# Kernel tuning notes

Measured on AMD Instinct MI355X. Metric: run time of the kernel, lower is better.

## Reference

```python
import jax, jax.numpy as jnp
import numpy as np

N_ATOMS = 50000
DEG = 16
N_EDGES = N_ATOMS * DEG
N_MOL = 1000
NA = 23  # NUMBER_ATOMIC_GRAPH_FEATURES
NB = 7   # NUMBER_BOND_GRAPH_FEATURES


def _sph(v):
    # e3nn-style real spherical harmonics, lmax=2, normalize=False, 'component' normalization
    x, y, z = v[:, 0], v[:, 1], v[:, 2]
    sh1 = jnp.sqrt(3.0) * jnp.stack([x, y, z], axis=-1)  # [E,3] (1o)
    sh2 = jnp.stack([
        jnp.sqrt(15.0) * x * y,
        jnp.sqrt(15.0) * y * z,
        (jnp.sqrt(5.0) / 2.0) * (2 * z * z - x * x - y * y),
        jnp.sqrt(15.0) * x * z,
        (jnp.sqrt(15.0) / 2.0) * (x * x - y * y),
    ], axis=-1)  # [E,5] (2e)
    return sh1, sh2


def setup_inputs() -> dict:
    key = jax.random.key(0)
    ks = jax.random.split(key, 10)
    positions = jax.random.normal(ks[0], (N_ATOMS, 3), jnp.float32)
    x = jax.random.normal(ks[1], (N_ATOMS, NA), jnp.float32)
    edge_attr = jax.random.uniform(ks[2], (N_EDGES, NB), jnp.float32)
    edge_src = jax.random.randint(ks[3], (N_EDGES,), 0, N_ATOMS)
    edge_dst = jnp.repeat(jnp.arange(N_ATOMS), DEG)  # every node has in-degree DEG (required by the module)
    batch = jnp.repeat(jnp.arange(N_MOL), N_ATOMS // N_MOL)
    # tp1: FullyConnectedTensorProduct(NAx0e, 7x0e+7x1o+7x2e -> 32x0e+12x1e+12x1o+8x2e+8x2o)
    # allowed paths: 0e*0e->0e (32), 0e*1o->1o (12), 0e*2e->2e (8); 1e/2o outputs have no path (zero)
    W1_0 = jax.random.normal(ks[4], (NA, NB, 32), jnp.float32)
    W1_1 = jax.random.normal(ks[5], (NA, NB, 12), jnp.float32)
    W1_2 = jax.random.normal(ks[6], (NA, NB, 8), jnp.float32)
    # tp2: paths into 0e: 0e*0e (32x7), 1o*1o (12x7), 2e*2e (8x7)
    W2_0 = jax.random.normal(ks[7], (32, NB, 1), jnp.float32)
    W2_1 = jax.random.normal(ks[8], (12, NB, 1), jnp.float32)
    W2_2 = jax.random.normal(ks[9], (8, NB, 1), jnp.float32)
    return {"positions": positions, "x": x, "edge_attr": edge_attr,
            "W1_0": W1_0, "W1_1": W1_1, "W1_2": W1_2,
            "W2_0": W2_0, "W2_1": W2_1, "W2_2": W2_2,
            "edge_src": edge_src, "edge_dst": edge_dst, "batch": batch}


def reference(positions, x, edge_attr, W1_0, W1_1, W1_2, W2_0, W2_1, W2_2, edge_src, edge_dst, batch):
    N = x.shape[0]
    E = edge_attr.shape[0]
    M = N_MOL
    vec = positions[edge_src] - positions[edge_dst]            # [E,3]
    sh1, sh2 = _sph(vec)
    # FullTensorProduct(7x0e, 0e+1o+2e): scalar block is edge_attr itself; l>0 blocks are outer products
    b1 = edge_attr[:, :, None] * sh1[:, None, :]               # [E,NB,3]
    b2 = edge_attr[:, :, None] * sh2[:, None, :]               # [E,NB,5]
    deg = jax.ops.segment_sum(jnp.ones((E,), positions.dtype), edge_dst, num_segments=N)
    inv_sqrt_deg = 1.0 / jnp.sqrt(deg)                          # all nodes have >=1 edge by construction
    # tp1 on gathered source atom scalars. Since in1 is all-scalar, the SH factor separates:
    t = x[edge_src][:, :, None] * edge_attr[:, None, :]         # [E,NA,NB]
    n1 = 1.0 / np.sqrt(NA * NB)                                 # fan-in normalization
    m0 = jnp.einsum('eab,abo->eo', t, W1_0) * n1                # [E,32] 0e
    m1 = (jnp.einsum('eab,abo->eo', t, W1_1) * n1)[:, :, None] * sh1[:, None, :]  # [E,12,3] 1o
    m2 = (jnp.einsum('eab,abo->eo', t, W1_2) * n1)[:, :, None] * sh2[:, None, :]  # [E,8,5] 2e
    # (tp1's 12x1e and 8x2o outputs are structurally zero and have no path into tp2's 0e output -> dropped)
    s0 = jax.ops.segment_sum(m0, edge_dst, num_segments=N) * inv_sqrt_deg[:, None]
    s1 = jax.ops.segment_sum(m1, edge_dst, num_segments=N) * inv_sqrt_deg[:, None, None]
    s2 = jax.ops.segment_sum(m2, edge_dst, num_segments=N) * inv_sqrt_deg[:, None, None]
    # tp2 -> single 0e; l x l -> 0 contraction is inner product / sqrt(2l+1)
    e0 = jnp.einsum('ea,eb,ab->e', s0[edge_src], edge_attr, W2_0[:, :, 0]) / np.sqrt(32 * NB)
    e1 = jnp.einsum('eam,ebm,ab->e', s1[edge_src], b1, W2_1[:, :, 0]) / (np.sqrt(12 * NB) * np.sqrt(3.0))
    e2 = jnp.einsum('eam,ebm,ab->e', s2[edge_src], b2, W2_2[:, :, 0]) / (np.sqrt(8 * NB) * np.sqrt(5.0))
    edge_out = (e0 + e1 + e2)[:, None]                          # [E,1]
    node_out = jax.ops.segment_sum(edge_out, edge_dst, num_segments=N) * inv_sqrt_deg[:, None]
    apm = jax.ops.segment_sum(jnp.ones((N,), positions.dtype), batch, num_segments=M)
    acc = jax.ops.segment_sum(node_out, batch, num_segments=M)  # [M,1]
    return acc / jnp.sqrt(apm)[:, None]
```

## Files before the change

kernel.cpp:

```cpp
#include <hip/hip_runtime.h>
#include <hip/hip_bf16.h>

#define N_ATOMS 50000
#define DEG 16
#define N_MOL 1000
#define NA 23
#define NB 7
#define O0 32
#define O1 12
#define O2 8
#define OT 52
#define SROW 128
#define NPW 4
#define WFRAG_N 1792

typedef __attribute__((ext_vector_type(8))) short short8;
typedef __attribute__((ext_vector_type(4))) float floatx4;

__device__ __forceinline__ unsigned short bfbits(float f) {
    unsigned u = __float_as_uint(f);
    u += 0x7FFFu + ((u >> 16) & 1u);
    return (unsigned short)(u >> 16);
}
__device__ __forceinline__ float bf_lo(unsigned u) { return __uint_as_float(u << 16); }
__device__ __forceinline__ float bf_hi(unsigned u) { return __uint_as_float(u & 0xFFFF0000u); }
__device__ __forceinline__ float wred4(float v) {
    v += __shfl_xor(v, 16, 64); v += __shfl_xor(v, 32, 64); return v;
}

__global__ void k_prep(const float* __restrict__ W1_0, const float* __restrict__ W1_1,
                       const float* __restrict__ W1_2, const float* __restrict__ x,
                       const float* __restrict__ pos,
                       unsigned short* __restrict__ Wfrag,
                       unsigned short* __restrict__ x_bf, float4* __restrict__ pos4,
                       float* __restrict__ out) {
    int idx = blockIdx.x * 256 + threadIdx.x;
    if (idx < N_MOL) out[idx] = 0.0f;
    if (idx < WFRAG_N * 8) {
        int j    = idx & 7;
        int lane = (idx >> 3) & 63;
        int st   = idx >> 9;
        int s = st >> 2, t = st & 3;
        int a = (lane >> 4) * 8 + j, o = t * 16 + (lane & 15);
        float val = 0.f;
        if (a < NA && o < OT) {
            const float n1 = 0.07881104062391006f;
            if (o < O0)           val = W1_0[(a * NB + s) * O0 + o] * n1;
            else if (o < O0 + O1) val = W1_1[(a * NB + s) * O1 + (o - O0)] * n1;
            else                  val = W1_2[(a * NB + s) * O2 + (o - O0 - O1)] * n1;
        }
        Wfrag[idx] = bfbits(val);
    }
    if (idx < N_ATOMS) {
        float4 p; p.x = pos[idx * 3 + 0]; p.y = pos[idx * 3 + 1];
        p.z = pos[idx * 3 + 2]; p.w = 0.f;
        pos4[idx] = p;
    }
    if (idx < N_ATOMS * 32) {
        int n = idx >> 5, a = idx & 31;
        x_bf[idx] = bfbits((a < NA) ? x[n * NA + a] : 0.f);
    }
}

__global__ __launch_bounds__(256, 5) void k2_s(const float4* __restrict__ pos4,
        const unsigned short* __restrict__ x_bf, const float* __restrict__ edge_attr,
        const int* __restrict__ edge_src, const unsigned short* __restrict__ Wfrag,
        unsigned short* __restrict__ sbuf) {
    __shared__ short8 wfrag[WFRAG_N];
    __shared__ float hbuf[4][16][8];
    const int tid  = threadIdx.x;
    const int wid  = tid >> 6;
    const int lane = tid & 63;
    const int lcol = lane & 15;
    const int quad = lane >> 4;

    {
        uint4* dst = (uint4*)wfrag;
        const uint4* src4 = (const uint4*)Wfrag;
        for (int i = tid; i < WFRAG_N; i += 256) dst[i] = src4[i];
    }
    __syncthreads();

    const int wgid = __builtin_amdgcn_readfirstlane(blockIdx.x * 4 + wid);
    const int base = wgid * NPW;
    if (base >= N_ATOMS) return;

    float (*hb)[8] = hbuf[wid];
    const float s3 = 1.7320508075688772f, s15 = 3.872983346207417f;
    const float s5h = 1.118033988749895f, s15h = 1.9364916731037085f;

    auto clampn = [&](int i) { int nn = base + i; return nn < N_ATOMS ? nn : N_ATOMS - 1; };
    int s0v = edge_src[clampn(0) * DEG + lcol];
    int s1v = edge_src[clampn(1) * DEG + lcol];
    uint4 xu0 = *(const uint4*)(x_bf + s0v * 32 + quad * 8);
    float4 pp0 = pos4[s0v];
    float e0v[NB];
    {
        const float* p = edge_attr + ((size_t)clampn(0) * DEG + lcol) * NB;
        #pragma unroll
        for (int b = 0; b < NB; b++) e0v[b] = p[b];
    }

    #pragma unroll 1
    for (int i = 0; i < NPW; i++) {
        const int n = base + i;
        if (n >= N_ATOMS) break;
        int s2v = edge_src[clampn(i + 2 < NPW ? i + 2 : i) * DEG + lcol];
        uint4 xu1 = *(const uint4*)(x_bf + s1v * 32 + quad * 8);
        float4 pp1 = pos4[s1v];
        float e1v[NB];
        {
            const float* p = edge_attr + ((size_t)clampn(i + 1 < NPW ? i + 1 : i) * DEG + lcol) * NB;
            #pragma unroll
            for (int b = 0; b < NB; b++) e1v[b] = p[b];
        }
        float xf[8];
        xf[0] = bf_lo(xu0.x); xf[1] = bf_hi(xu0.x);
        xf[2] = bf_lo(xu0.y); xf[3] = bf_hi(xu0.y);
        xf[4] = bf_lo(xu0.z); xf[5] = bf_hi(xu0.z);
        xf[6] = bf_lo(xu0.w); xf[7] = bf_hi(xu0.w);

        const float4 pd = pos4[n];
        if (lane < 16) {
            const float vx = pp0.x - pd.x, vy = pp0.y - pd.y, vz = pp0.z - pd.z;
            hb[lane][0] = s3 * vx;  hb[lane][1] = s3 * vy;  hb[lane][2] = s3 * vz;
            hb[lane][3] = s15 * vx * vy;
            hb[lane][4] = s15 * vy * vz;
            hb[lane][5] = s5h * (2.f * vz * vz - vx * vx - vy * vy);
            hb[lane][6] = s15 * vx * vz;
            hb[lane][7] = s15h * (vx * vx - vy * vy);
        }
        floatx4 acc0 = {0.f,0.f,0.f,0.f}, acc1 = {0.f,0.f,0.f,0.f};
        floatx4 acc2 = {0.f,0.f,0.f,0.f}, acc3 = {0.f,0.f,0.f,0.f};
        #pragma unroll
        for (int s = 0; s < 7; s++) {
            const float eb = e0v[s];
            union { short8 v; unsigned u[4]; } af;
            #pragma unroll
            for (int j = 0; j < 8; j += 2) {
                float2 pr; pr.x = xf[j] * eb; pr.y = xf[j + 1] * eb;
                __hip_bfloat162 bb = __float22bfloat162_rn(pr);
                af.u[j >> 1] = *(unsigned*)&bb;
            }
            acc0 = __builtin_amdgcn_mfma_f32_16x16x32_bf16(af.v, wfrag[(s*4+0)*64 + lane], acc0, 0, 0, 0);
            acc1 = __builtin_amdgcn_mfma_f32_16x16x32_bf16(af.v, wfrag[(s*4+1)*64 + lane], acc1, 0, 0, 0);
            acc2 = __builtin_amdgcn_mfma_f32_16x16x32_bf16(af.v, wfrag[(s*4+2)*64 + lane], acc2, 0, 0, 0);
            acc3 = __builtin_amdgcn_mfma_f32_16x16x32_bf16(af.v, wfrag[(s*4+3)*64 + lane], acc3, 0, 0, 0);
        }
        float4 hA[4], hB[4];
        #pragma unroll
        for (int r = 0; r < 4; r++) {
            int e = quad * 4 + r;
            hA[r] = *(const float4*)&hb[e][0];
            hB[r] = *(const float4*)&hb[e][4];
        }
        const float q = 0.25f;
        unsigned short* sr = sbuf + (size_t)n * SROW;
        float v0 = wred4(acc0[0] + acc0[1] + acc0[2] + acc0[3]);
        float v1 = wred4(acc1[0] + acc1[1] + acc1[2] + acc1[3]);
        if (quad == 0) { sr[lcol] = bfbits(v0 * q); sr[16 + lcol] = bfbits(v1 * q); }
        if (lcol < 12) {
            float t0 = 0.f, t1 = 0.f, t2 = 0.f;
            #pragma unroll
            for (int r = 0; r < 4; r++) {
                float m = acc2[r];
                t0 += m * hA[r].x; t1 += m * hA[r].y; t2 += m * hA[r].z;
            }
            t0 = wred4(t0); t1 = wred4(t1); t2 = wred4(t2);
            if (quad == 0) {
                sr[32 + lcol] = bfbits(t0 * q);
                sr[44 + lcol] = bfbits(t1 * q);
                sr[56 + lcol] = bfbits(t2 * q);
            }
        } else {
            int a = lcol - 12;
            float t0 = 0.f, t1 = 0.f, t2 = 0.f, t3 = 0.f, t4 = 0.f;
            #pragma unroll
            for (int r = 0; r < 4; r++) {
                float m = acc2[r];
                t0 += m * hA[r].w; t1 += m * hB[r].x; t2 += m * hB[r].y;
                t3 += m * hB[r].z; t4 += m * hB[r].w;
            }
            t0 = wred4(t0); t1 = wred4(t1); t2 = wred4(t2); t3 = wred4(t3); t4 = wred4(t4);
            if (quad == 0) {
                sr[68 + a] = bfbits(t0 * q); sr[76 + a] = bfbits(t1 * q);
                sr[84 + a] = bfbits(t2 * q); sr[92 + a] = bfbits(t3 * q);
                sr[100 + a] = bfbits(t4 * q);
            }
        }
        if (lcol < 4) {
            int a = lcol + 4;
            float t0 = 0.f, t1 = 0.f, t2 = 0.f, t3 = 0.f, t4 = 0.f;
            #pragma unroll
            for (int r = 0; r < 4; r++) {
                float m = acc3[r];
                t0 += m * hA[r].w; t1 += m * hB[r].x; t2 += m * hB[r].y;
                t3 += m * hB[r].z; t4 += m * hB[r].w;
            }
            t0 = wred4(t0); t1 = wred4(t1); t2 = wred4(t2); t3 = wred4(t3); t4 = wred4(t4);
            if (quad == 0) {
                sr[68 + a] = bfbits(t0 * q); sr[76 + a] = bfbits(t1 * q);
                sr[84 + a] = bfbits(t2 * q); sr[92 + a] = bfbits(t3 * q);
                sr[100 + a] = bfbits(t4 * q);
            }
        }
        s0v = s1v; s1v = s2v;
        xu0 = xu1; pp0 = pp1;
        #pragma unroll
        for (int b = 0; b < NB; b++) e0v[b] = e1v[b];
    }
}

__global__ __launch_bounds__(256, 7) void k3_fused(const float4* __restrict__ pos4,
        const float* __restrict__ edge_attr, const int* __restrict__ edge_src,
        const unsigned short* __restrict__ sbuf,
        const float* __restrict__ W2_0, const float* __restrict__ W2_1,
        const float* __restrict__ W2_2, float* __restrict__ out) {
    __shared__ float ea_t[4][4][16][8];
    __shared__ float hbf[4][4][161];
    const int tid  = threadIdx.x;
    const int wid  = tid >> 6;
    const int lane = tid & 63;
    const int q    = lane >> 4;
    const int e    = lane & 15;
    const int base = __builtin_amdgcn_readfirstlane(blockIdx.x * 4 + wid) * 4;

    const float c0 = 0.06681531047810609f;
    const float c1 = 0.06299407883487121f;
    const float c2 = 0.05976143046671968f;
    int code = 0, aA = 0, aB = 0, valid = 1;
    const float* Wb = W2_0; float norm = c0;
    const int j = lane;
    if (j < 16)      { code = 0; aA = 2 * j;   aB = aA + 1; Wb = W2_0; norm = c0; }
    else if (j < 34) { int g = (j - 16) / 6, r = (j - 16) - 6 * g;
                       code = 1 + g; aA = 2 * r; aB = aA + 1; Wb = W2_1; norm = c1; }
    else if (j < 54) { int g = (j - 34) >> 2, r = (j - 34) & 3;
                       code = 4 + g; aA = 2 * r; aB = aA + 1; Wb = W2_2; norm = c2; }
    else             { valid = 0; }
    float wA[NB], wB[NB];
    #pragma unroll
    for (int b = 0; b < NB; b++) {
        wA[b] = valid ? Wb[aA * NB + b] * norm : 0.f;
        wB[b] = valid ? Wb[aB * NB + b] * norm : 0.f;
    }
    const int jj = valid ? j : 0;

    {
        const int nq = base + q;
        const int sE = edge_src[nq * DEG + e];
        const float* eap = edge_attr + ((size_t)nq * DEG + e) * NB;
        float ev[8];
        #pragma unroll
        for (int b = 0; b < NB; b++) ev[b] = eap[b];
        ev[7] = 0.f;
        const float4 ps = pos4[sE];
        const float4 pd = pos4[nq];
        const float vx = ps.x - pd.x, vy = ps.y - pd.y, vz = ps.z - pd.z;
        float* ed = &ea_t[wid][q][e][0];
        *(float4*)(ed)     = *(float4*)&ev[0];
        *(float4*)(ed + 4) = *(float4*)&ev[4];
        const float s3 = 1.7320508075688772f, s15 = 3.872983346207417f;
        const float s5h = 1.118033988749895f, s15h = 1.9364916731037085f;
        float* hr = &hbf[wid][q][e * 10];
        hr[0] = 1.0f;
        hr[1] = s3 * vx; hr[2] = s3 * vy; hr[3] = s3 * vz;
        hr[4] = s15 * vx * vy;
        hr[5] = s15 * vy * vz;
        hr[6] = s5h * (2.f * vz * vz - vx * vx - vy * vy);
        hr[7] = s15 * vx * vz;
        hr[8] = s15h * (vx * vx - vy * vy);
    }

    const int* srcp = edge_src + (size_t)base * DEG;
    unsigned g0[DEG], g1[DEG];
    #pragma unroll
    for (int k = 0; k < DEG; k++) {
        int s = __builtin_amdgcn_readfirstlane(srcp[k]);
        g0[k] = *(const unsigned*)(sbuf + (size_t)s * SROW + 2 * jj);
    }
    #pragma unroll
    for (int i = 0; i < 4; i++) {
        if (i + 1 < 4) {
            #pragma unroll
            for (int k = 0; k < DEG; k++) {
                int s = __builtin_amdgcn_readfirstlane(srcp[(i + 1) * DEG + k]);
                g1[k] = *(const unsigned*)(sbuf + (size_t)s * SROW + 2 * jj);
            }
        }
        const float* hw = &hbf[wid][i][0];
        float acc = 0.f;
        #pragma unroll
        for (int k = 0; k < DEG; k++) {
            const float4 eA = *(const float4*)&ea_t[wid][i][k][0];
            const float4 eB = *(const float4*)&ea_t[wid][i][k][4];
            const float f = hw[k * 10 + code];
            float we0 = eA.x * wA[0] + eA.y * wA[1] + eA.z * wA[2] + eA.w * wA[3]
                      + eB.x * wA[4] + eB.y * wA[5] + eB.z * wA[6];
            float we1 = eA.x * wB[0] + eA.y * wB[1] + eA.z * wB[2] + eA.w * wB[3]
                      + eB.x * wB[4] + eB.y * wB[5] + eB.z * wB[6];
            acc += f * (bf_lo(g0[k]) * we0 + bf_hi(g0[k]) * we1);
        }
        acc = valid ? acc : 0.f;
        #pragma unroll
        for (int off = 32; off >= 1; off >>= 1) acc += __shfl_xor(acc, off, 64);
        if (lane == 0)
            atomicAdd(out + ((base + i) / 50), acc * 0.035355339059327376f);
        #pragma unroll
        for (int k = 0; k < DEG; k++) g0[k] = g1[k];
    }
}

extern "C" void kernel_launch(void* const* d_in, const int* in_sizes, int n_in,
                              void* d_out, int out_size, void* d_ws, size_t ws_size,
                              hipStream_t stream) {
    const float* pos  = (const float*)d_in[0];
    const float* x    = (const float*)d_in[1];
    const float* ea   = (const float*)d_in[2];
    const float* W1_0 = (const float*)d_in[3];
    const float* W1_1 = (const float*)d_in[4];
    const float* W1_2 = (const float*)d_in[5];
    const float* W2_0 = (const float*)d_in[6];
    const float* W2_1 = (const float*)d_in[7];
    const float* W2_2 = (const float*)d_in[8];
    const int*   esrc = (const int*)d_in[9];
    float* out = (float*)d_out;

    char* ws = (char*)d_ws;
    unsigned short* Wfrag = (unsigned short*)ws;
    unsigned short* sbuf  = (unsigned short*)(ws + 32768);
    unsigned short* x_bf  = (unsigned short*)(ws + 32768 + 12800000);
    float4*         pos4  = (float4*)(ws + 32768 + 12800000 + 3200000);

    hipLaunchKernelGGL(k_prep, dim3((N_ATOMS * 32 + 255) / 256), dim3(256), 0, stream,
                       W1_0, W1_1, W1_2, x, pos, Wfrag, x_bf, pos4, out);
    hipLaunchKernelGGL(k2_s, dim3((N_ATOMS / NPW + 3) / 4), dim3(256), 0, stream,
                       pos4, x_bf, ea, esrc, Wfrag, sbuf);
    hipLaunchKernelGGL(k3_fused, dim3(N_ATOMS / 16), dim3(256), 0, stream,
                       pos4, ea, esrc, sbuf, W2_0, W2_1, W2_2, out);
}
```

Measured before the change: 208.5 us.

## Fold W2 into W1 weights to shrink per-node intermediate and simplify edge pass

Precomputes the product of the tp1 and tp2 weight tensors in the prep kernel, so the node stage produces a compact 21-channel-by-harmonic intermediate instead of the full 52-channel irreps. The MFMA count in the node kernel halves (two output tiles instead of four), and the intermediate is stored as a 64-float row per node. The edge kernel becomes a simple per-edge dot product with spherical harmonics and edge attributes, one wave per node, with no shared-memory staging. The costs are fp32 storage of the intermediate (same byte size as before) and reassociated arithmetic, which changes rounding.

```diff
diff --git a/kernel.cpp b/kernel.cpp
--- a/kernel.cpp
+++ b/kernel.cpp
@@ -9,10 +9,11 @@
 #define O0 32
 #define O1 12
 #define O2 8
-#define OT 52
-#define SROW 128
+#define OZ 21
+#define NT 2
+#define ZROW 64
 #define NPW 4
-#define WFRAG_N 1792
+#define VFRAG_N 896
 
 typedef __attribute__((ext_vector_type(8))) short short8;
 typedef __attribute__((ext_vector_type(4))) float floatx4;
@@ -29,27 +30,44 @@
 }
 
 __global__ void k_prep(const float* __restrict__ W1_0, const float* __restrict__ W1_1,
-                       const float* __restrict__ W1_2, const float* __restrict__ x,
-                       const float* __restrict__ pos,
-                       unsigned short* __restrict__ Wfrag,
+                       const float* __restrict__ W1_2,
+                       const float* __restrict__ W2_0, const float* __restrict__ W2_1,
+                       const float* __restrict__ W2_2,
+                       const float* __restrict__ x, const float* __restrict__ pos,
+                       unsigned short* __restrict__ Vfrag,
                        unsigned short* __restrict__ x_bf, float4* __restrict__ pos4,
                        float* __restrict__ out) {
     int idx = blockIdx.x * 256 + threadIdx.x;
     if (idx < N_MOL) out[idx] = 0.0f;
-    if (idx < WFRAG_N * 8) {
+    if (idx < VFRAG_N * 8) {
         int j    = idx & 7;
         int lane = (idx >> 3) & 63;
         int st   = idx >> 9;
-        int s = st >> 2, t = st & 3;
+        int s = st >> 1, t = st & 1;
         int a = (lane >> 4) * 8 + j, o = t * 16 + (lane & 15);
         float val = 0.f;
-        if (a < NA && o < OT) {
+        if (a < NA && o < OZ) {
             const float n1 = 0.07881104062391006f;
-            if (o < O0)           val = W1_0[(a * NB + s) * O0 + o] * n1;
-            else if (o < O0 + O1) val = W1_1[(a * NB + s) * O1 + (o - O0)] * n1;
-            else                  val = W1_2[(a * NB + s) * O2 + (o - O0 - O1)] * n1;
-        }
-        Wfrag[idx] = bfbits(val);
+            const float q  = 0.25f;
+            float acc = 0.f;
+            if (o < 7) {
+                const float c0 = 0.06681531047810609f;
+                const float* w1 = W1_0 + (a * NB + s) * O0;
+                for (int k = 0; k < O0; k++) acc += w1[k] * W2_0[k * NB + o];
+                val = acc * (n1 * c0 * q);
+            } else if (o < 14) {
+                const float c1 = 0.06299407883487121f;
+                const float* w1 = W1_1 + (a * NB + s) * O1;
+                for (int k = 0; k < O1; k++) acc += w1[k] * W2_1[k * NB + (o - 7)];
+                val = acc * (n1 * c1 * q);
+            } else {
+                const float c2 = 0.05976143046671968f;
+                const float* w1 = W1_2 + (a * NB + s) * O2;
+                for (int k = 0; k < O2; k++) acc += w1[k] * W2_2[k * NB + (o - 14)];
+                val = acc * (n1 * c2 * q);
+            }
+        }
+        Vfrag[idx] = bfbits(val);
     }
     if (idx < N_ATOMS) {
         float4 p; p.x = pos[idx * 3 + 0]; p.y = pos[idx * 3 + 1];
@@ -64,9 +82,9 @@
 
 __global__ __launch_bounds__(256, 5) void k2_s(const float4* __restrict__ pos4,
         const unsigned short* __restrict__ x_bf, const float* __restrict__ edge_attr,
-        const int* __restrict__ edge_src, const unsigned short* __restrict__ Wfrag,
-        unsigned short* __restrict__ sbuf) {
-    __shared__ short8 wfrag[WFRAG_N];
+        const int* __restrict__ edge_src, const unsigned short* __restrict__ Vfrag,
+        float* __restrict__ zbuf) {
+    __shared__ short8 wfrag[VFRAG_N];
     __shared__ float hbuf[4][16][8];
     const int tid  = threadIdx.x;
     const int wid  = tid >> 6;
@@ -76,8 +94,8 @@
 
     {
         uint4* dst = (uint4*)wfrag;
-        const uint4* src4 = (const uint4*)Wfrag;
-        for (int i = tid; i < WFRAG_N; i += 256) dst[i] = src4[i];
+        const uint4* src4 = (const uint4*)Vfrag;
+        for (int i = tid; i < VFRAG_N; i += 256) dst[i] = src4[i];
     }
     __syncthreads();
 
@@ -131,7 +149,6 @@
             hb[lane][7] = s15h * (vx * vx - vy * vy);
         }
         floatx4 acc0 = {0.f,0.f,0.f,0.f}, acc1 = {0.f,0.f,0.f,0.f};
-        floatx4 acc2 = {0.f,0.f,0.f,0.f}, acc3 = {0.f,0.f,0.f,0.f};
         #pragma unroll
         for (int s = 0; s < 7; s++) {
             const float eb = e0v[s];
@@ -142,10 +159,8 @@
                 __hip_bfloat162 bb = __float22bfloat162_rn(pr);
                 af.u[j >> 1] = *(unsigned*)&bb;
             }
-            acc0 = __builtin_amdgcn_mfma_f32_16x16x32_bf16(af.v, wfrag[(s*4+0)*64 + lane], acc0, 0, 0, 0);
-            acc1 = __builtin_amdgcn_mfma_f32_16x16x32_bf16(af.v, wfrag[(s*4+1)*64 + lane], acc1, 0, 0, 0);
-            acc2 = __builtin_amdgcn_mfma_f32_16x16x32_bf16(af.v, wfrag[(s*4+2)*64 + lane], acc2, 0, 0, 0);
-            acc3 = __builtin_amdgcn_mfma_f32_16x16x32_bf16(af.v, wfrag[(s*4+3)*64 + lane], acc3, 0, 0, 0);
+            acc0 = __builtin_amdgcn_mfma_f32_16x16x32_bf16(af.v, wfrag[(s*NT+0)*64 + lane], acc0, 0, 0, 0);
+            acc1 = __builtin_amdgcn_mfma_f32_16x16x32_bf16(af.v, wfrag[(s*NT+1)*64 + lane], acc1, 0, 0, 0);
         }
         float4 hA[4], hB[4];
         #pragma unroll
@@ -154,55 +169,34 @@
             hA[r] = *(const float4*)&hb[e][0];
             hB[r] = *(const float4*)&hb[e][4];
         }
-        const float q = 0.25f;
-        unsigned short* sr = sbuf + (size_t)n * SROW;
-        float v0 = wred4(acc0[0] + acc0[1] + acc0[2] + acc0[3]);
-        float v1 = wred4(acc1[0] + acc1[1] + acc1[2] + acc1[3]);
-        if (quad == 0) { sr[lcol] = bfbits(v0 * q); sr[16 + lcol] = bfbits(v1 * q); }
-        if (lcol < 12) {
-            float t0 = 0.f, t1 = 0.f, t2 = 0.f;
-            #pragma unroll
-            for (int r = 0; r < 4; r++) {
-                float m = acc2[r];
-                t0 += m * hA[r].x; t1 += m * hA[r].y; t2 += m * hA[r].z;
-            }
-            t0 = wred4(t0); t1 = wred4(t1); t2 = wred4(t2);
-            if (quad == 0) {
-                sr[32 + lcol] = bfbits(t0 * q);
-                sr[44 + lcol] = bfbits(t1 * q);
-                sr[56 + lcol] = bfbits(t2 * q);
-            }
-        } else {
-            int a = lcol - 12;
-            float t0 = 0.f, t1 = 0.f, t2 = 0.f, t3 = 0.f, t4 = 0.f;
-            #pragma unroll
-            for (int r = 0; r < 4; r++) {
-                float m = acc2[r];
-                t0 += m * hA[r].w; t1 += m * hB[r].x; t2 += m * hB[r].y;
-                t3 += m * hB[r].z; t4 += m * hB[r].w;
-            }
-            t0 = wred4(t0); t1 = wred4(t1); t2 = wred4(t2); t3 = wred4(t3); t4 = wred4(t4);
-            if (quad == 0) {
-                sr[68 + a] = bfbits(t0 * q); sr[76 + a] = bfbits(t1 * q);
-                sr[84 + a] = bfbits(t2 * q); sr[92 + a] = bfbits(t3 * q);
-                sr[100 + a] = bfbits(t4 * q);
-            }
-        }
-        if (lcol < 4) {
-            int a = lcol + 4;
-            float t0 = 0.f, t1 = 0.f, t2 = 0.f, t3 = 0.f, t4 = 0.f;
-            #pragma unroll
-            for (int r = 0; r < 4; r++) {
-                float m = acc3[r];
-                t0 += m * hA[r].w; t1 += m * hB[r].x; t2 += m * hB[r].y;
-                t3 += m * hB[r].z; t4 += m * hB[r].w;
-            }
-            t0 = wred4(t0); t1 = wred4(t1); t2 = wred4(t2); t3 = wred4(t3); t4 = wred4(t4);
-            if (quad == 0) {
-                sr[68 + a] = bfbits(t0 * q); sr[76 + a] = bfbits(t1 * q);
-                sr[84 + a] = bfbits(t2 * q); sr[92 + a] = bfbits(t3 * q);
-                sr[100 + a] = bfbits(t4 * q);
-            }
+        float* sr = zbuf + (size_t)n * ZROW;
+        const bool useA = (lcol >= 14);
+        float v0 = acc0[0] + acc0[1] + acc0[2] + acc0[3];
+        float u0 = 0.f, u1 = 0.f, u2 = 0.f;
+        float t0 = 0.f, t1 = 0.f, t2 = 0.f, t3 = 0.f, t4 = 0.f;
+        #pragma unroll
+        for (int r = 0; r < 4; r++) {
+            float m0 = acc0[r], m1 = acc1[r];
+            u0 += m0 * hA[r].x; u1 += m0 * hA[r].y; u2 += m0 * hA[r].z;
+            float mz = useA ? m0 : m1;
+            t0 += mz * hA[r].w; t1 += mz * hB[r].x; t2 += mz * hB[r].y;
+            t3 += mz * hB[r].z; t4 += mz * hB[r].w;
+        }
+        v0 = wred4(v0);
+        u0 = wred4(u0); u1 = wred4(u1); u2 = wred4(u2);
+        t0 = wred4(t0); t1 = wred4(t1); t2 = wred4(t2); t3 = wred4(t3); t4 = wred4(t4);
+        if (quad == 0) {
+            if (lcol < 7) sr[lcol * 8] = v0;
+            else if (lcol < 14) {
+                int b = lcol - 7;
+                sr[b * 8 + 1] = u0; sr[b * 8 + 2] = u1; sr[b * 8 + 3] = u2;
+            }
+            if (lcol >= 14 || lcol < 5) {
+                int b = useA ? (lcol - 14) : (lcol + 2);
+                sr[b * 8 + 4] = t0; sr[b * 8 + 5] = t1; sr[b * 8 + 6] = t2;
+                sr[b * 8 + 7] = t3; sr[56 + b] = t4;
+            }
+            if (lcol == 5) sr[63] = 0.f;
         }
         s0v = s1v; s1v = s2v;
         xu0 = xu1; pp0 = pp1;
@@ -211,103 +205,47 @@
     }
 }
 
-__global__ __launch_bounds__(256, 7) void k3_fused(const float4* __restrict__ pos4,
+__global__ __launch_bounds__(256, 8) void k3_fused(const float4* __restrict__ pos4,
         const float* __restrict__ edge_attr, const int* __restrict__ edge_src,
-        const unsigned short* __restrict__ sbuf,
-        const float* __restrict__ W2_0, const float* __restrict__ W2_1,
-        const float* __restrict__ W2_2, float* __restrict__ out) {
-    __shared__ float ea_t[4][4][16][8];
-    __shared__ float hbf[4][4][161];
+        const float* __restrict__ zbuf, float* __restrict__ out) {
     const int tid  = threadIdx.x;
     const int wid  = tid >> 6;
     const int lane = tid & 63;
-    const int q    = lane >> 4;
-    const int e    = lane & 15;
-    const int base = __builtin_amdgcn_readfirstlane(blockIdx.x * 4 + wid) * 4;
-
-    const float c0 = 0.06681531047810609f;
-    const float c1 = 0.06299407883487121f;
-    const float c2 = 0.05976143046671968f;
-    int code = 0, aA = 0, aB = 0, valid = 1;
-    const float* Wb = W2_0; float norm = c0;
-    const int j = lane;
-    if (j < 16)      { code = 0; aA = 2 * j;   aB = aA + 1; Wb = W2_0; norm = c0; }
-    else if (j < 34) { int g = (j - 16) / 6, r = (j - 16) - 6 * g;
-                       code = 1 + g; aA = 2 * r; aB = aA + 1; Wb = W2_1; norm = c1; }
-    else if (j < 54) { int g = (j - 34) >> 2, r = (j - 34) & 3;
-                       code = 4 + g; aA = 2 * r; aB = aA + 1; Wb = W2_2; norm = c2; }
-    else             { valid = 0; }
-    float wA[NB], wB[NB];
+    const int n = __builtin_amdgcn_readfirstlane(blockIdx.x * 4 + wid);
+    const int k = lane >> 2, r = lane & 3;
+
+    const int s = edge_src[n * DEG + k];
+    const float* zr = zbuf + (size_t)s * ZROW;
+    const float* zp = zr + 16 * r;
+    float4 Z0 = *(const float4*)(zp);
+    float4 Z1 = *(const float4*)(zp + 4);
+    float4 Z2 = *(const float4*)(zp + 8);
+    float4 Z3 = *(const float4*)(zp + 12);
+    float2 C8 = *(const float2*)(zr + 56 + 2 * r);
+    const float* eap = edge_attr + ((size_t)n * DEG + k) * NB;
+    float ea0 = eap[2 * r];
+    float ea1 = (r < 3) ? eap[2 * r + 1] : 0.f;
+
+    float4 ps = pos4[s];
+    float4 pd = pos4[n];
+    const float vx = ps.x - pd.x, vy = ps.y - pd.y, vz = ps.z - pd.z;
+    const float s3 = 1.7320508075688772f, s15 = 3.872983346207417f;
+    const float s5h = 1.118033988749895f, s15h = 1.9364916731037085f;
+    const float h1 = s3 * vx, h2 = s3 * vy, h3 = s3 * vz;
+    const float h4 = s15 * vx * vy, h5 = s15 * vy * vz;
+    const float h6 = s5h * (2.f * vz * vz - vx * vx - vy * vy);
+    const float h7 = s15 * vx * vz, h8 = s15h * (vx * vx - vy * vy);
+
+    float t0 = Z0.x + h1 * Z0.y + h2 * Z0.z + h3 * Z0.w
+             + h4 * Z1.x + h5 * Z1.y + h6 * Z1.z + h7 * Z1.w + h8 * C8.x;
+    float t1 = Z2.x + h1 * Z2.y + h2 * Z2.z + h3 * Z2.w
+             + h4 * Z3.x + h5 * Z3.y + h6 * Z3.z + h7 * Z3.w + h8 * C8.y;
+    float acc = ea0 * t0 + ea1 * t1;
+
     #pragma unroll
-    for (int b = 0; b < NB; b++) {
-        wA[b] = valid ? Wb[aA * NB + b] * norm : 0.f;
-        wB[b] = valid ? Wb[aB * NB + b] * norm : 0.f;
-    }
-    const int jj = valid ? j : 0;
-
-    {
-        const int nq = base + q;
-        const int sE = edge_src[nq * DEG + e];
-        const float* eap = edge_attr + ((size_t)nq * DEG + e) * NB;
-        float ev[8];
-        #pragma unroll
-        for (int b = 0; b < NB; b++) ev[b] = eap[b];
-        ev[7] = 0.f;
-        const float4 ps = pos4[sE];
-        const float4 pd = pos4[nq];
-        const float vx = ps.x - pd.x, vy = ps.y - pd.y, vz = ps.z - pd.z;
-        float* ed = &ea_t[wid][q][e][0];
-        *(float4*)(ed)     = *(float4*)&ev[0];
-        *(float4*)(ed + 4) = *(float4*)&ev[4];
-        const float s3 = 1.7320508075688772f, s15 = 3.872983346207417f;
-        const float s5h = 1.118033988749895f, s15h = 1.9364916731037085f;
-        float* hr = &hbf[wid][q][e * 10];
-        hr[0] = 1.0f;
-        hr[1] = s3 * vx; hr[2] = s3 * vy; hr[3] = s3 * vz;
-        hr[4] = s15 * vx * vy;
-        hr[5] = s15 * vy * vz;
-        hr[6] = s5h * (2.f * vz * vz - vx * vx - vy * vy);
-        hr[7] = s15 * vx * vz;
-        hr[8] = s15h * (vx * vx - vy * vy);
-    }
-
-    const int* srcp = edge_src + (size_t)base * DEG;
-    unsigned g0[DEG], g1[DEG];
-    #pragma unroll
-    for (int k = 0; k < DEG; k++) {
-        int s = __builtin_amdgcn_readfirstlane(srcp[k]);
-        g0[k] = *(const unsigned*)(sbuf + (size_t)s * SROW + 2 * jj);
-    }
-    #pragma unroll
-    for (int i = 0; i < 4; i++) {
-        if (i + 1 < 4) {
-            #pragma unroll
-            for (int k = 0; k < DEG; k++) {
-                int s = __builtin_amdgcn_readfirstlane(srcp[(i + 1) * DEG + k]);
-                g1[k] = *(const unsigned*)(sbuf + (size_t)s * SROW + 2 * jj);
-            }
-        }
-        const float* hw = &hbf[wid][i][0];
-        float acc = 0.f;
-        #pragma unroll
-        for (int k = 0; k < DEG; k++) {
-            const float4 eA = *(const float4*)&ea_t[wid][i][k][0];
-            const float4 eB = *(const float4*)&ea_t[wid][i][k][4];
-            const float f = hw[k * 10 + code];
-            float we0 = eA.x * wA[0] + eA.y * wA[1] + eA.z * wA[2] + eA.w * wA[3]
-                      + eB.x * wA[4] + eB.y * wA[5] + eB.z * wA[6];
-            float we1 = eA.x * wB[0] + eA.y * wB[1] + eA.z * wB[2] + eA.w * wB[3]
-                      + eB.x * wB[4] + eB.y * wB[5] + eB.z * wB[6];
-            acc += f * (bf_lo(g0[k]) * we0 + bf_hi(g0[k]) * we1);
-        }
-        acc = valid ? acc : 0.f;
-        #pragma unroll
-        for (int off = 32; off >= 1; off >>= 1) acc += __shfl_xor(acc, off, 64);
-        if (lane == 0)
-            atomicAdd(out + ((base + i) / 50), acc * 0.035355339059327376f);
-        #pragma unroll
-        for (int k = 0; k < DEG; k++) g0[k] = g1[k];
-    }
+    for (int off = 32; off >= 1; off >>= 1) acc += __shfl_xor(acc, off, 64);
+    if (lane == 0)
+        atomicAdd(out + n / 50, acc * 0.035355339059327376f);
 }
 
 extern "C" void kernel_launch(void* const* d_in, const int* in_sizes, int n_in,
@@ -326,15 +264,15 @@
     float* out = (float*)d_out;
 
     char* ws = (char*)d_ws;
-    unsigned short* Wfrag = (unsigned short*)ws;
-    unsigned short* sbuf  = (unsigned short*)(ws + 32768);
+    unsigned short* Vfrag = (unsigned short*)ws;
+    float*          zbuf  = (float*)(ws + 32768);
     unsigned short* x_bf  = (unsigned short*)(ws + 32768 + 12800000);
     float4*         pos4  = (float4*)(ws + 32768 + 12800000 + 3200000);
 
     hipLaunchKernelGGL(k_prep, dim3((N_ATOMS * 32 + 255) / 256), dim3(256), 0, stream,
-                       W1_0, W1_1, W1_2, x, pos, Wfrag, x_bf, pos4, out);
+                       W1_0, W1_1, W1_2, W2_0, W2_1, W2_2, x, pos, Vfrag, x_bf, pos4, out);
     hipLaunchKernelGGL(k2_s, dim3((N_ATOMS / NPW + 3) / 4), dim3(256), 0, stream,
-                       pos4, x_bf, ea, esrc, Wfrag, sbuf);
-    hipLaunchKernelGGL(k3_fused, dim3(N_ATOMS / 16), dim3(256), 0, stream,
-                       pos4, ea, esrc, sbuf, W2_0, W2_1, W2_2, out);
-}
+                       pos4, x_bf, ea, esrc, Vfrag, zbuf);
+    hipLaunchKernelGGL(k3_fused, dim3(N_ATOMS / 4), dim3(256), 0, stream,
+                       pos4, ea, esrc, zbuf, out);
+}
```

After: 188.9 us. 1.1x faster.
